# Optimization experiments

Measured on AMD Instinct MI355X. Metric: run time of the kernel, lower is better.

The kernel has to match this reference:

```python
import jax, jax.numpy as jnp
import numpy as np

B, S, D, H = 4, 2048, 1024, 16
HD = D // H  # head_dim = 64


def setup_inputs() -> dict:
    key = jax.random.key(0)
    ks = jax.random.split(key, 10)
    scale = 1.0 / np.sqrt(D)
    x = jax.random.normal(ks[0], (B, S, D), dtype=jnp.float32)
    mask = jax.random.randint(ks[1], (B, S, S), 0, 2, dtype=jnp.int32)
    Wq = jax.random.normal(ks[2], (D, D), dtype=jnp.float32) * scale
    Wk = jax.random.normal(ks[3], (D, D), dtype=jnp.float32) * scale
    Wv = jax.random.normal(ks[4], (D, D), dtype=jnp.float32) * scale
    Wo = jax.random.normal(ks[5], (D, D), dtype=jnp.float32) * scale
    bq = jax.random.normal(ks[6], (D,), dtype=jnp.float32) * 0.01
    bk = jax.random.normal(ks[7], (D,), dtype=jnp.float32) * 0.01
    bv = jax.random.normal(ks[8], (D,), dtype=jnp.float32) * 0.01
    bo = jax.random.normal(ks[9], (D,), dtype=jnp.float32) * 0.01
    return {"x": x, "mask": mask, "Wq": Wq, "bq": bq, "Wk": Wk, "bk": bk,
            "Wv": Wv, "bv": bv, "Wo": Wo, "bo": bo}


def reference(x, mask, Wq, bq, Wk, bk, Wv, bv, Wo, bo):
    # QKV projections (nn.Linear: x @ W^T + b; W stored pre-transposed here as [D,D])
    q = x @ Wq + bq  # [B,S,D]
    k = x @ Wk + bk
    v = x @ Wv + bv
    # split heads -> [B,H,S,HD]
    def heads(t):
        return t.reshape(B, S, H, HD).transpose(0, 2, 1, 3)
    q, k, v = heads(q), heads(k), heads(v)
    scores = jnp.einsum('bhqd,bhkd->bhqk', q, k) / jnp.sqrt(jnp.float32(HD))
    # mask: [B,S,S] -> broadcast over heads; positions where mask==0 get -inf
    scores = jnp.where(mask[:, None, :, :] == 0, -jnp.inf, scores)
    attn = jax.nn.softmax(scores, axis=-1)
    attn = jnp.where(jnp.isnan(attn), 0.0, attn)  # nan_to_num(nan=0.0)
    out = jnp.einsum('bhqk,bhkd->bhqd', attn, v)  # [B,H,S,HD]
    out = out.transpose(0, 2, 1, 3).reshape(B, S, D)
    return out @ Wo + bo
```

## Files before the change

kernel.cpp:

```cpp
#include <hip/hip_runtime.h>
#include <hip/hip_bf16.h>
#include <stdint.h>

#define B_  4
#define S_  2048
#define D_  1024
#define H_  16
#define HD_ 64

typedef __attribute__((ext_vector_type(4))) float f32x4;
typedef __attribute__((ext_vector_type(8))) short bf16x8;

typedef const unsigned int __attribute__((address_space(1)))* gas_ptr;
typedef unsigned int __attribute__((address_space(3)))* las_ptr;

__device__ __forceinline__ void async16(const void* g, void* l) {
  __builtin_amdgcn_global_load_lds((gas_ptr)g, (las_ptr)l, 16, 0, 0);
}

__global__ __launch_bounds__(256) void cvt_x(const float* __restrict__ in,
                                             __hip_bfloat16* __restrict__ out,
                                             int n) {
  const int i = (blockIdx.x * blockDim.x + threadIdx.x) * 4;
  if (i >= n) return;
  const float4 v = *(const float4*)(in + i);
  union { ushort4 u; __hip_bfloat16 h[4]; } o;
  o.h[0] = (__hip_bfloat16)v.x;
  o.h[1] = (__hip_bfloat16)v.y;
  o.h[2] = (__hip_bfloat16)v.z;
  o.h[3] = (__hip_bfloat16)v.w;
  *(ushort4*)(out + i) = o.u;
}

__global__ __launch_bounds__(256) void expand_mask(const int* __restrict__ mk,
                                                   uint2* __restrict__ xm) {
  const unsigned j = blockIdx.x * 256 + threadIdx.x;
  const int mt = j & 3, lane = (j >> 2) & 63, kt = (j >> 8) & 31;
  const int qg = j >> 13;
  const int quad = lane >> 4, l16 = lane & 15;
  const size_t row = (size_t)qg * 16 + l16;
  const int key = kt * 64 + mt * 16 + quad * 4;
  const int4 m = *(const int4*)(mk + row * 2048 + key);
  uint2 o;
  o.x = (m.x ? 0xFFFFu : 0u) | (m.y ? 0xFFFF0000u : 0u);
  o.y = (m.z ? 0xFFFFu : 0u) | (m.w ? 0xFFFF0000u : 0u);
  xm[j] = o;
}

__global__ void transpose_w(const float* __restrict__ Wq,
                            const float* __restrict__ Wk,
                            const float* __restrict__ Wv,
                            const float* __restrict__ Wo,
                            __hip_bfloat16* __restrict__ Wt_qkv,
                            __hip_bfloat16* __restrict__ Wt_o) {
  __shared__ float t[32][33];
  const int z = blockIdx.z;
  const float* W = (z == 0) ? Wq : (z == 1) ? Wk : (z == 2) ? Wv : Wo;
  __hip_bfloat16* Wt = (z < 3) ? (Wt_qkv + (size_t)z * D_ * D_) : Wt_o;
  const int x = blockIdx.x * 32 + threadIdx.x;
  const int y = blockIdx.y * 32 + threadIdx.y;
  t[threadIdx.y][threadIdx.x] = W[(size_t)y * D_ + x];
  __syncthreads();
  const int xo = blockIdx.y * 32 + threadIdx.x;
  const int yo = blockIdx.x * 32 + threadIdx.y;
  Wt[(size_t)yo * D_ + xo] = (__hip_bfloat16)t[threadIdx.x][threadIdx.y];
}

__global__ __launch_bounds__(256) void gemm_qkv(
    const __hip_bfloat16* __restrict__ A,
    const __hip_bfloat16* __restrict__ Bt,
    const float* __restrict__ bq,
    const float* __restrict__ bk,
    const float* __restrict__ bv,
    __hip_bfloat16* __restrict__ QKo,
    __hip_bfloat16* __restrict__ Vt) {
  __shared__ __hip_bfloat16 sA[128 * 64];
  __shared__ __hip_bfloat16 sB[128 * 64];
  const int K = 1024;
  const int tid  = threadIdx.x;
  const int wave = tid >> 6;
  const int lane = tid & 63;
  const int quad = lane >> 4;
  const int l16  = lane & 15;
  const int wg  = blockIdx.x;
  const int swz = (wg & 7) * 192 + (wg >> 3);
  const int bm = (swz / 24) * 128;
  const int bn = (swz % 24) * 128;
  const int wm = (wave >> 1) * 64;
  const int wn = (wave & 1) * 64;

  const int srow = lane >> 3;
  const int schk = (lane & 7) ^ srow;
  const __hip_bfloat16* gA = A  + (size_t)(bm + wave * 32 + srow) * K + schk * 8;
  const __hip_bfloat16* gB = Bt + (size_t)(bn + wave * 32 + srow) * K + schk * 8;
  char* const lA = (char*)sA + wave * 32 * 128;
  char* const lB = (char*)sB + wave * 32 * 128;

  const int xl = l16 & 7;
  const int koff = (quad ^ xl) * 16;
  const char* pa = (const char*)sA + (wm + l16) * 128;
  const char* pb = (const char*)sB + (wn + l16) * 128;

  f32x4 acc[4][4] = {};

  for (int k0 = 0; k0 < K; k0 += 64) {
#pragma unroll
    for (int t = 0; t < 4; ++t) {
      async16(gA + (size_t)(t * 8) * K + k0, lA + t * 1024);
      async16(gB + (size_t)(t * 8) * K + k0, lB + t * 1024);
    }
    __syncthreads();
#pragma unroll
    for (int c = 0; c < 2; ++c) {
      const int off = koff ^ (c * 64);
      bf16x8 af[4], bf[4];
#pragma unroll
      for (int mt = 0; mt < 4; ++mt) af[mt] = *(const bf16x8*)(pa + mt * 2048 + off);
#pragma unroll
      for (int nt = 0; nt < 4; ++nt) bf[nt] = *(const bf16x8*)(pb + nt * 2048 + off);
#pragma unroll
      for (int mt = 0; mt < 4; ++mt)
#pragma unroll
        for (int nt = 0; nt < 4; ++nt)
          acc[mt][nt] = __builtin_amdgcn_mfma_f32_16x16x32_bf16(af[mt], bf[nt], acc[mt][nt], 0, 0, 0);
    }
    __syncthreads();
  }

#pragma unroll
  for (int mt = 0; mt < 4; ++mt) {
    const int row = bm + wm + mt * 16 + quad * 4;
#pragma unroll
    for (int nt = 0; nt < 4; ++nt) {
      const int col = bn + wn + nt * 16 + l16;
      f32x4 v = acc[mt][nt];
      if (col < 2048) {
        const float bias = (col < 1024) ? bq[col] : bk[col - 1024];
        const float sc = (col < 1024) ? 0.18033688011f : 1.0f;
#pragma unroll
        for (int r = 0; r < 4; ++r)
          QKo[(size_t)(row + r) * 2048 + col] = (__hip_bfloat16)((v[r] + bias) * sc);
      } else {
        const int cv = col - 2048;
        const float bias = bv[cv];
        const int hh = cv >> 6, d = cv & 63;
        const int bb = row >> 11, s0 = row & 2047;
        union { __hip_bfloat16 h[4]; unsigned long long u; } pk;
#pragma unroll
        for (int r = 0; r < 4; ++r) pk.h[r] = (__hip_bfloat16)(v[r] + bias);
        *(unsigned long long*)(Vt + ((size_t)(bb * 16 + hh) * 64 + d) * 2048 + s0) = pk.u;
      }
    }
  }
}

__global__ __launch_bounds__(256) void gemm_out(
    const __hip_bfloat16* __restrict__ A,
    const __hip_bfloat16* __restrict__ Bt,
    const float* __restrict__ b0,
    float* __restrict__ C,
    int N, int K) {
  __shared__ __hip_bfloat16 sA[128 * 64];
  __shared__ __hip_bfloat16 sB[128 * 64];
  const int tid  = threadIdx.x;
  const int wave = tid >> 6;
  const int lane = tid & 63;
  const int quad = lane >> 4;
  const int l16  = lane & 15;
  const int wg  = blockIdx.x;
  const int swz = (wg & 7) * 64 + (wg >> 3);
  const int bm = (swz >> 3) * 128;
  const int bn = (swz & 7) * 128;
  const int wm = (wave >> 1) * 64;
  const int wn = (wave & 1) * 64;

  const int srow = lane >> 3;
  const int schk = (lane & 7) ^ srow;
  const __hip_bfloat16* gA = A  + (size_t)(bm + wave * 32 + srow) * K + schk * 8;
  const __hip_bfloat16* gB = Bt + (size_t)(bn + wave * 32 + srow) * K + schk * 8;
  char* const lA = (char*)sA + wave * 32 * 128;
  char* const lB = (char*)sB + wave * 32 * 128;

  const int xl = l16 & 7;
  const int koff = (quad ^ xl) * 16;
  const char* pa = (const char*)sA + (wm + l16) * 128;
  const char* pb = (const char*)sB + (wn + l16) * 128;

  f32x4 acc[4][4] = {};

  for (int k0 = 0; k0 < K; k0 += 64) {
#pragma unroll
    for (int t = 0; t < 4; ++t) {
      async16(gA + (size_t)(t * 8) * K + k0, lA + t * 1024);
      async16(gB + (size_t)(t * 8) * K + k0, lB + t * 1024);
    }
    __syncthreads();
#pragma unroll
    for (int c = 0; c < 2; ++c) {
      const int off = koff ^ (c * 64);
      bf16x8 af[4], bf[4];
#pragma unroll
      for (int mt = 0; mt < 4; ++mt) af[mt] = *(const bf16x8*)(pa + mt * 2048 + off);
#pragma unroll
      for (int nt = 0; nt < 4; ++nt) bf[nt] = *(const bf16x8*)(pb + nt * 2048 + off);
#pragma unroll
      for (int mt = 0; mt < 4; ++mt)
#pragma unroll
        for (int nt = 0; nt < 4; ++nt)
          acc[mt][nt] = __builtin_amdgcn_mfma_f32_16x16x32_bf16(af[mt], bf[nt], acc[mt][nt], 0, 0, 0);
    }
    __syncthreads();
  }

#pragma unroll
  for (int mt = 0; mt < 4; ++mt) {
    const int row = bm + wm + mt * 16 + quad * 4;
#pragma unroll
    for (int nt = 0; nt < 4; ++nt) {
      const int col = bn + wn + nt * 16 + l16;
      const float bias = b0[col];
      f32x4 v = acc[mt][nt];
#pragma unroll
      for (int r = 0; r < 4; ++r)
        C[(size_t)(row + r) * N + col] = v[r] + bias;
    }
  }
}

__global__ __launch_bounds__(256, 4) void flash_attn(
    const __hip_bfloat16* __restrict__ QK,
    const __hip_bfloat16* __restrict__ Vt,
    const uint4* __restrict__ XM,
    __hip_bfloat16* __restrict__ O) {
  __shared__ __hip_bfloat16 sK[2][64 * 64];
  __shared__ __hip_bfloat16 sV[2][64 * 64];

  const int qt = blockIdx.x, h = blockIdx.y, b = blockIdx.z;
  const int tid = threadIdx.x;
  const int wave = tid >> 6, lane = tid & 63, quad = lane >> 4, l16 = lane & 15;
  const int qbase = qt * 128;
  const size_t brow = (size_t)b * S_;
  const int bh = b * H_ + h;

  bf16x8 qf[2][2];
#pragma unroll
  for (int g = 0; g < 2; ++g) {
    const __hip_bfloat16* qrow =
        QK + (brow + qbase + g * 64 + wave * 16 + l16) * 2048 + h * 64;
#pragma unroll
    for (int c = 0; c < 2; ++c)
      qf[g][c] = *(const bf16x8*)(qrow + c * 32 + quad * 8);
  }

  const int srow = lane >> 3;
  const int schk = (lane & 7) ^ srow;
  const __hip_bfloat16* gk0 =
      QK + (brow + wave * 16 + srow) * 2048 + 1024 + h * 64 + schk * 8;
  const __hip_bfloat16* gk1 = gk0 + (size_t)8 * 2048;
  const __hip_bfloat16* gv0 =
      Vt + ((size_t)bh * 64 + wave * 16 + srow) * 2048 + schk * 8;
  const __hip_bfloat16* gv1 = gv0 + (size_t)8 * 2048;
  char* const lK[2] = {(char*)&sK[0][0] + wave * 2048, (char*)&sK[1][0] + wave * 2048};
  char* const lV[2] = {(char*)&sV[0][0] + wave * 2048, (char*)&sV[1][0] + wave * 2048};

  const uint4* xpa =
      XM + ((size_t)(b * 128 + qt * 8 + wave) * 32) * 128 + (size_t)lane * 2;
  const uint4* xpb = xpa + (size_t)4 * 32 * 128;

  const int xl = l16 & 7;
  const int koff0 = ((quad ^ xl) * 16);
  const int rowb = l16 * 128;

  const bf16x8 onesv = {(short)0x3F80, (short)0x3F80, (short)0x3F80, (short)0x3F80,
                        (short)0x3F80, (short)0x3F80, (short)0x3F80, (short)0x3F80};
  f32x4 lacc[2] = {};
  f32x4 oacc[2][4] = {};

  async16(gk0, lK[0]);
  async16(gk1, lK[0] + 1024);
  async16(gv0, lV[0]);
  async16(gv1, lV[0] + 1024);
  gk0 += (size_t)64 * 2048; gk1 += (size_t)64 * 2048;
  gv0 += 64; gv1 += 64;
  __syncthreads();

  const int NT = S_ / 64;
  for (int kt = 0; kt < NT; ++kt) {
    const int cur = kt & 1, nxt = cur ^ 1;

    if (kt + 1 < NT) {
      async16(gk0, lK[nxt]);
      async16(gk1, lK[nxt] + 1024);
      async16(gv0, lV[nxt]);
      async16(gv1, lV[nxt] + 1024);
      gk0 += (size_t)64 * 2048; gk1 += (size_t)64 * 2048;
      gv0 += 64; gv1 += 64;
    }
    const uint4 ca0 = xpa[(size_t)kt * 128];
    const uint4 ca1 = xpa[(size_t)kt * 128 + 1];
    const uint4 cb0 = xpb[(size_t)kt * 128];
    const uint4 cb1 = xpb[(size_t)kt * 128 + 1];

    const char* bK = (const char*)&sK[cur][0] + rowb;
    unsigned pl[2][4][2];
    __builtin_amdgcn_s_setprio(1);
#pragma unroll
    for (int mt = 0; mt < 4; ++mt) {
      const bf16x8 kf0 = *(const bf16x8*)(bK + mt * 2048 + koff0);
      const bf16x8 kf1 = *(const bf16x8*)(bK + mt * 2048 + (koff0 ^ 64));
      f32x4 a0 = {}, a1 = {};
      a0 = __builtin_amdgcn_mfma_f32_16x16x32_bf16(kf0, qf[0][0], a0, 0, 0, 0);
      a0 = __builtin_amdgcn_mfma_f32_16x16x32_bf16(kf1, qf[0][1], a0, 0, 0, 0);
      a1 = __builtin_amdgcn_mfma_f32_16x16x32_bf16(kf0, qf[1][0], a1, 0, 0, 0);
      a1 = __builtin_amdgcn_mfma_f32_16x16x32_bf16(kf1, qf[1][1], a1, 0, 0, 0);
#pragma unroll
      for (int g = 0; g < 2; ++g) {
        const uint4 cc = g ? ((mt < 2) ? cb0 : cb1) : ((mt < 2) ? ca0 : ca1);
        const unsigned w0 = (mt & 1) ? cc.z : cc.x;
        const unsigned w1 = (mt & 1) ? cc.w : cc.y;
        const f32x4 av = g ? a1 : a0;
        union { __hip_bfloat16 h[2]; unsigned u; } c0, c1;
        c0.h[0] = (__hip_bfloat16)__builtin_amdgcn_exp2f(av[0]);
        c0.h[1] = (__hip_bfloat16)__builtin_amdgcn_exp2f(av[1]);
        c1.h[0] = (__hip_bfloat16)__builtin_amdgcn_exp2f(av[2]);
        c1.h[1] = (__hip_bfloat16)__builtin_amdgcn_exp2f(av[3]);
        pl[g][mt][0] = c0.u & w0;
        pl[g][mt][1] = c1.u & w1;
      }
    }
    __builtin_amdgcn_s_setprio(0);

    bf16x8 pf[2][2];
#pragma unroll
    for (int g = 0; g < 2; ++g)
#pragma unroll
      for (int c = 0; c < 2; ++c) {
        unsigned e0 = pl[g][2 * c][0], o0 = pl[g][2 * c + 1][0];
        unsigned e1 = pl[g][2 * c][1], o1 = pl[g][2 * c + 1][1];
        asm("v_permlane32_swap_b32 %0, %1" : "+v"(e0), "+v"(o0));
        asm("v_permlane16_swap_b32 %0, %1" : "+v"(e0), "+v"(o0));
        asm("v_permlane32_swap_b32 %0, %1" : "+v"(e1), "+v"(o1));
        asm("v_permlane16_swap_b32 %0, %1" : "+v"(e1), "+v"(o1));
        union { unsigned u[4]; bf16x8 v; } uu;
        uu.u[0] = e0; uu.u[1] = e1; uu.u[2] = o0; uu.u[3] = o1;
        pf[g][c] = uu.v;
      }

    const char* bV = (const char*)&sV[cur][0] + rowb;
    __builtin_amdgcn_s_setprio(1);
#pragma unroll
    for (int ht = 0; ht < 4; ++ht) {
      const bf16x8 vf0 = *(const bf16x8*)(bV + ht * 2048 + koff0);
      const bf16x8 vf1 = *(const bf16x8*)(bV + ht * 2048 + (koff0 ^ 64));
      oacc[0][ht] = __builtin_amdgcn_mfma_f32_16x16x32_bf16(vf0, pf[0][0], oacc[0][ht], 0, 0, 0);
      oacc[0][ht] = __builtin_amdgcn_mfma_f32_16x16x32_bf16(vf1, pf[0][1], oacc[0][ht], 0, 0, 0);
      oacc[1][ht] = __builtin_amdgcn_mfma_f32_16x16x32_bf16(vf0, pf[1][0], oacc[1][ht], 0, 0, 0);
      oacc[1][ht] = __builtin_amdgcn_mfma_f32_16x16x32_bf16(vf1, pf[1][1], oacc[1][ht], 0, 0, 0);
    }
    lacc[0] = __builtin_amdgcn_mfma_f32_16x16x32_bf16(onesv, pf[0][0], lacc[0], 0, 0, 0);
    lacc[0] = __builtin_amdgcn_mfma_f32_16x16x32_bf16(onesv, pf[0][1], lacc[0], 0, 0, 0);
    lacc[1] = __builtin_amdgcn_mfma_f32_16x16x32_bf16(onesv, pf[1][0], lacc[1], 0, 0, 0);
    lacc[1] = __builtin_amdgcn_mfma_f32_16x16x32_bf16(onesv, pf[1][1], lacc[1], 0, 0, 0);
    __builtin_amdgcn_s_setprio(0);

    __syncthreads();
  }

#pragma unroll
  for (int g = 0; g < 2; ++g) {
    const float l = lacc[g][0];
    const float inv = (l > 0.f) ? 1.f / l : 0.f;
    __hip_bfloat16* orow =
        O + (brow + qbase + g * 64 + wave * 16 + l16) * 1024 + h * 64;
#pragma unroll
    for (int ht = 0; ht < 4; ++ht) {
      union { __hip_bfloat16 h[4]; unsigned long long u; } ok_;
#pragma unroll
      for (int r = 0; r < 4; ++r) ok_.h[r] = (__hip_bfloat16)(oacc[g][ht][r] * inv);
      *(unsigned long long*)(orow + ht * 16 + quad * 4) = ok_.u;
    }
  }
}

extern "C" void kernel_launch(void* const* d_in, const int* in_sizes, int n_in,
                              void* d_out, int out_size, void* d_ws, size_t ws_size,
                              hipStream_t stream) {
  const float* x  = (const float*)d_in[0];
  const int*   mk = (const int*)d_in[1];
  const float* Wq = (const float*)d_in[2];
  const float* bq = (const float*)d_in[3];
  const float* Wk = (const float*)d_in[4];
  const float* bk = (const float*)d_in[5];
  const float* Wv = (const float*)d_in[6];
  const float* bv = (const float*)d_in[7];
  const float* Wo = (const float*)d_in[8];
  const float* bo = (const float*)d_in[9];
  float* out = (float*)d_out;

  __hip_bfloat16* X16    = (__hip_bfloat16*)d_ws;
  __hip_bfloat16* Wt_qkv = X16 + (size_t)B_ * S_ * D_;
  __hip_bfloat16* Wt_o   = Wt_qkv + (size_t)3 * D_ * D_;
  __hip_bfloat16* QK     = Wt_o + (size_t)D_ * D_;
  __hip_bfloat16* Vt     = QK + (size_t)B_ * S_ * 2 * D_;
  __hip_bfloat16* Obuf   = Vt + (size_t)B_ * H_ * HD_ * S_;
  unsigned* xmask = (unsigned*)(Obuf + (size_t)B_ * S_ * D_);

  const int nx = B_ * S_ * D_;
  cvt_x<<<dim3((nx / 4 + 255) / 256), 256, 0, stream>>>(x, X16, nx);
  transpose_w<<<dim3(32, 32, 4), dim3(32, 32), 0, stream>>>(Wq, Wk, Wv, Wo, Wt_qkv, Wt_o);
  expand_mask<<<dim3((int)((size_t)B_ * S_ * S_ / 4 / 256)), 256, 0, stream>>>(
      mk, (uint2*)xmask);
  gemm_qkv<<<dim3(24 * 64), 256, 0, stream>>>(
      X16, Wt_qkv, bq, bk, bv, QK, Vt);
  flash_attn<<<dim3(S_ / 128, H_, B_), 256, 0, stream>>>(
      QK, Vt, (const uint4*)xmask, Obuf);
  gemm_out<<<dim3(8 * 64), 256, 0, stream>>>(
      Obuf, Wt_o, bo, out, D_, D_);
}
```

Measured before the change: 358.0 us.

## Rewrite QKV GEMM as 256x256 double-buffered, 8-wave pipelined kernel

The QKV projection GEMM now uses 256x256 output tiles with 512 threads (8 waves) and double-buffered LDS. Async global-to-LDS loads for the next K tiles are interleaved with MFMA quadrants, using explicit barriers, waitcnts and s_setprio. The aim is to hide memory latency and raise arithmetic intensity per tile compared with the single-buffered 128x128 loop. The cost is heavier register use (128 accumulator floats per lane), 128 KB of LDS per workgroup, and fragile hand-built synchronisation.

Result: slower. 368.0 us (+2.8%).

```diff
diff --git a/kernel.cpp b/kernel.cpp
--- a/kernel.cpp
+++ b/kernel.cpp
@@ -66,7 +66,44 @@
   Wt[(size_t)yo * D_ + xo] = (__hip_bfloat16)t[threadIdx.x][threadIdx.y];
 }
 
-__global__ __launch_bounds__(256) void gemm_qkv(
+__device__ __forceinline__ f32x4 mfma16(bf16x8 a, bf16x8 b, f32x4 c) {
+  return __builtin_amdgcn_mfma_f32_16x16x32_bf16(a, b, c, 0, 0, 0);
+}
+
+template<int MH>
+__device__ __forceinline__ void rdA(const char* base, int koff, bf16x8 (&af)[2][2]) {
+#pragma unroll
+  for (int m = 0; m < 2; ++m)
+#pragma unroll
+    for (int kc = 0; kc < 2; ++kc)
+      af[m][kc] = *(const bf16x8*)(base + (MH * 2 + m) * 2048 + (koff ^ (kc * 64)));
+}
+
+template<int NH>
+__device__ __forceinline__ void rdB(const char* base, int koff, bf16x8 (&bf)[4][2]) {
+#pragma unroll
+  for (int n = 0; n < 4; ++n)
+#pragma unroll
+    for (int kc = 0; kc < 2; ++kc)
+      bf[n][kc] = *(const bf16x8*)(base + (NH * 4 + n) * 2048 + (koff ^ (kc * 64)));
+}
+
+template<int MH, int NH>
+__device__ __forceinline__ void mm16(const bf16x8 (&af)[2][2], const bf16x8 (&bf)[4][2],
+                                     f32x4 (&acc)[4][8]) {
+  __builtin_amdgcn_s_setprio(1);
+#pragma unroll
+  for (int m = 0; m < 2; ++m)
+#pragma unroll
+    for (int n = 0; n < 4; ++n)
+#pragma unroll
+      for (int kc = 0; kc < 2; ++kc)
+        acc[MH * 2 + m][NH * 4 + n] =
+            mfma16(af[m][kc], bf[n][kc], acc[MH * 2 + m][NH * 4 + n]);
+  __builtin_amdgcn_s_setprio(0);
+}
+
+__global__ __launch_bounds__(512, 2) void gemm_qkv(
     const __hip_bfloat16* __restrict__ A,
     const __hip_bfloat16* __restrict__ Bt,
     const float* __restrict__ bq,
@@ -74,64 +111,94 @@
     const float* __restrict__ bv,
     __hip_bfloat16* __restrict__ QKo,
     __hip_bfloat16* __restrict__ Vt) {
-  __shared__ __hip_bfloat16 sA[128 * 64];
-  __shared__ __hip_bfloat16 sB[128 * 64];
-  const int K = 1024;
-  const int tid  = threadIdx.x;
-  const int wave = tid >> 6;
-  const int lane = tid & 63;
-  const int quad = lane >> 4;
-  const int l16  = lane & 15;
+  __shared__ __hip_bfloat16 sA[2][256 * 64];
+  __shared__ __hip_bfloat16 sB[2][256 * 64];
+  const int t512 = threadIdx.x;
+  const int wave = t512 >> 6, lane = t512 & 63, quad = lane >> 4, l16 = lane & 15;
   const int wg  = blockIdx.x;
-  const int swz = (wg & 7) * 192 + (wg >> 3);
-  const int bm = (swz / 24) * 128;
-  const int bn = (swz % 24) * 128;
+  const int swz = (wg & 7) * 48 + (wg >> 3);
+  const int bm = (swz / 12) * 256;
+  const int bn = (swz % 12) * 256;
   const int wm = (wave >> 1) * 64;
-  const int wn = (wave & 1) * 64;
-
-  const int srow = lane >> 3;
-  const int schk = (lane & 7) ^ srow;
-  const __hip_bfloat16* gA = A  + (size_t)(bm + wave * 32 + srow) * K + schk * 8;
-  const __hip_bfloat16* gB = Bt + (size_t)(bn + wave * 32 + srow) * K + schk * 8;
-  char* const lA = (char*)sA + wave * 32 * 128;
-  char* const lB = (char*)sB + wave * 32 * 128;
+  const int wn = (wave & 1) * 128;
+
+  const int schk = (t512 & 7) ^ ((t512 >> 3) & 7);
+  const __hip_bfloat16* gA = A  + ((size_t)bm + (t512 >> 3)) * 1024 + schk * 8;
+  const __hip_bfloat16* gB = Bt + ((size_t)bn + (t512 >> 3)) * 1024 + schk * 8;
+  char* const lA[2] = {(char*)&sA[0][0] + wave * 1024, (char*)&sA[1][0] + wave * 1024};
+  char* const lB[2] = {(char*)&sB[0][0] + wave * 1024, (char*)&sB[1][0] + wave * 1024};
+
+#define STG(GP, LP, R0, KT) \
+  async16(GP + (size_t)(R0) * 1024 + (KT) * 64, LP + (R0) * 128)
+#define UA0(bf_, kt_) { STG(gA, lA[bf_], 0,   kt_); STG(gA, lA[bf_], 64,  kt_); }
+#define UA1(bf_, kt_) { STG(gA, lA[bf_], 128, kt_); STG(gA, lA[bf_], 192, kt_); }
+#define UB0(bf_, kt_) { STG(gB, lB[bf_], 0,   kt_); STG(gB, lB[bf_], 128, kt_); }
+#define UB1(bf_, kt_) { STG(gB, lB[bf_], 64,  kt_); STG(gB, lB[bf_], 192, kt_); }
+#define BAR  __builtin_amdgcn_s_barrier()
+#define LGKM0 { asm volatile("s_waitcnt lgkmcnt(0)" ::: "memory"); \
+                __builtin_amdgcn_sched_barrier(0); }
 
   const int xl = l16 & 7;
   const int koff = (quad ^ xl) * 16;
-  const char* pa = (const char*)sA + (wm + l16) * 128;
-  const char* pb = (const char*)sB + (wn + l16) * 128;
-
-  f32x4 acc[4][4] = {};
-
-  for (int k0 = 0; k0 < K; k0 += 64) {
-#pragma unroll
-    for (int t = 0; t < 4; ++t) {
-      async16(gA + (size_t)(t * 8) * K + k0, lA + t * 1024);
-      async16(gB + (size_t)(t * 8) * K + k0, lB + t * 1024);
-    }
-    __syncthreads();
-#pragma unroll
-    for (int c = 0; c < 2; ++c) {
-      const int off = koff ^ (c * 64);
-      bf16x8 af[4], bf[4];
-#pragma unroll
-      for (int mt = 0; mt < 4; ++mt) af[mt] = *(const bf16x8*)(pa + mt * 2048 + off);
-#pragma unroll
-      for (int nt = 0; nt < 4; ++nt) bf[nt] = *(const bf16x8*)(pb + nt * 2048 + off);
-#pragma unroll
-      for (int mt = 0; mt < 4; ++mt)
-#pragma unroll
-        for (int nt = 0; nt < 4; ++nt)
-          acc[mt][nt] = __builtin_amdgcn_mfma_f32_16x16x32_bf16(af[mt], bf[nt], acc[mt][nt], 0, 0, 0);
-    }
-    __syncthreads();
+  const char* rA[2] = {(char*)&sA[0][0] + (wm + l16) * 128,
+                       (char*)&sA[1][0] + (wm + l16) * 128};
+  const char* rB[2] = {(char*)&sB[0][0] + (wn + l16) * 128,
+                       (char*)&sB[1][0] + (wn + l16) * 128};
+
+  bf16x8 af[2][2], bfr[4][2];
+  f32x4 acc[4][8] = {};
+
+  UB0(0, 0); UB1(0, 0); UA0(0, 0); UA1(0, 0);
+  UB0(1, 1);
+  asm volatile("s_waitcnt vmcnt(2)" ::: "memory");
+  __builtin_amdgcn_sched_barrier(0);
+  BAR;
+  __builtin_amdgcn_sched_barrier(0);
+
+#pragma unroll 1
+  for (int it = 0; it < 8; ++it) {
+    const int k1 = 2 * it + 1, k2 = 2 * it + 2, k3 = 2 * it + 3;
+    const bool st = (it < 7);
+    rdB<0>(rB[0], koff, bfr); rdA<0>(rA[0], koff, af);
+    UB1(1, k1);
+    BAR; LGKM0; mm16<0, 0>(af, bfr, acc); BAR;
+    rdA<1>(rA[0], koff, af);
+    UA0(1, k1);
+    BAR; LGKM0; mm16<1, 0>(af, bfr, acc); BAR;
+    rdB<1>(rB[0], koff, bfr);
+    UA1(1, k1);
+    BAR; LGKM0; mm16<1, 1>(af, bfr, acc); BAR;
+    rdA<0>(rA[0], koff, af);
+    if (st) UB0(0, k2);
+    BAR; LGKM0; mm16<0, 1>(af, bfr, acc);
+    if (st) { asm volatile("s_waitcnt vmcnt(2)" ::: "memory"); }
+    else    { asm volatile("s_waitcnt vmcnt(0)" ::: "memory"); }
+    __builtin_amdgcn_sched_barrier(0);
+    BAR;
+    __builtin_amdgcn_sched_barrier(0);
+    rdB<0>(rB[1], koff, bfr); rdA<0>(rA[1], koff, af);
+    if (st) UB1(0, k2);
+    BAR; LGKM0; mm16<0, 0>(af, bfr, acc); BAR;
+    rdA<1>(rA[1], koff, af);
+    if (st) UA0(0, k2);
+    BAR; LGKM0; mm16<1, 0>(af, bfr, acc); BAR;
+    rdB<1>(rB[1], koff, bfr);
+    if (st) UA1(0, k2);
+    BAR; LGKM0; mm16<1, 1>(af, bfr, acc); BAR;
+    rdA<0>(rA[1], koff, af);
+    if (st) UB0(1, k3);
+    BAR; LGKM0; mm16<0, 1>(af, bfr, acc);
+    if (st) { asm volatile("s_waitcnt vmcnt(2)" ::: "memory"); }
+    __builtin_amdgcn_sched_barrier(0);
+    BAR;
+    __builtin_amdgcn_sched_barrier(0);
   }
 
 #pragma unroll
   for (int mt = 0; mt < 4; ++mt) {
     const int row = bm + wm + mt * 16 + quad * 4;
 #pragma unroll
-    for (int nt = 0; nt < 4; ++nt) {
+    for (int nt = 0; nt < 8; ++nt) {
       const int col = bn + wn + nt * 16 + l16;
       f32x4 v = acc[mt][nt];
       if (col < 2048) {
@@ -152,6 +219,13 @@
       }
     }
   }
+#undef STG
+#undef UA0
+#undef UA1
+#undef UB0
+#undef UB1
+#undef BAR
+#undef LGKM0
 }
 
 __global__ __launch_bounds__(256) void gemm_out(
@@ -410,7 +484,7 @@
   transpose_w<<<dim3(32, 32, 4), dim3(32, 32), 0, stream>>>(Wq, Wk, Wv, Wo, Wt_qkv, Wt_o);
   expand_mask<<<dim3((int)((size_t)B_ * S_ * S_ / 4 / 256)), 256, 0, stream>>>(
       mk, (uint2*)xmask);
-  gemm_qkv<<<dim3(24 * 64), 256, 0, stream>>>(
+  gemm_qkv<<<dim3(384), 512, 0, stream>>>(
       X16, Wt_qkv, bq, bk, bv, QK, Vt);
   flash_attn<<<dim3(S_ / 128, H_, B_), 256, 0, stream>>>(
       QK, Vt, (const uint4*)xmask, Obuf);
```
